# Kernel tuning notes

Hardware: AMD Instinct MI355X
Metric: run time of the kernel (lower is better)

## Reference

```python
import jax, jax.numpy as jnp
import numpy as np

SEQ, B, IN, H = 2048, 4096, 1, 32


def setup_inputs() -> dict:
    key = jax.random.key(0)
    ks = jax.random.split(key, 8)
    s_ih = 1.0 / np.sqrt(H)  # torch nn.RNN init scale
    return {
        "x": jax.random.normal(ks[0], (SEQ, B, IN), dtype=jnp.float32),
        "hidden": jnp.zeros((1, B, H), dtype=jnp.float32),
        "W_ih": jax.random.uniform(ks[1], (H, IN), jnp.float32, -s_ih, s_ih),
        "b_ih": jax.random.uniform(ks[2], (H,), jnp.float32, -s_ih, s_ih),
        "W_hh": jax.random.uniform(ks[3], (H, H), jnp.float32, -s_ih, s_ih),
        "b_hh": jax.random.uniform(ks[4], (H,), jnp.float32, -s_ih, s_ih),
        "W_fc": jax.random.uniform(ks[5], (IN, H), jnp.float32, -s_ih, s_ih),
        "b_fc": jax.random.uniform(ks[6], (IN,), jnp.float32, -s_ih, s_ih),
    }


def reference(x, hidden, W_ih, b_ih, W_hh, b_hh, W_fc, b_fc):
    # Elman RNN: h_t = tanh(x_t W_ih^T + b_ih + h_{t-1} W_hh^T + b_hh)
    # Precompute the input projection for all timesteps in one GEMM.
    x_proj = jnp.einsum('sbi,hi->sbh', x, W_ih) + b_ih + b_hh  # (SEQ, B, H)
    h0 = hidden[0]  # (B, H), single layer

    def step(h, xp_t):
        h_new = jnp.tanh(xp_t + h @ W_hh.T)
        return h_new, h_new

    _, outputs = jax.lax.scan(step, h0, x_proj)  # outputs: (SEQ, B, H)
    # Trailing Linear: (SEQ, B, H) -> (SEQ, B, IN)
    return jnp.einsum('sbh,oh->sbo', outputs, W_fc) + b_fc
```

## Files before the change

kernel.cpp:

```cpp
#include <hip/hip_runtime.h>

#define SEQ   2048
#define BATCH 4096
#define HD    32

__device__ __forceinline__ float exp2_fast(float a) {
#if __has_builtin(__builtin_amdgcn_exp2f)
    return __builtin_amdgcn_exp2f(a);
#else
    return exp2f(a);
#endif
}

__device__ __forceinline__ float rcp_fast(float a) {
#if __has_builtin(__builtin_amdgcn_rcpf)
    return __builtin_amdgcn_rcpf(a);
#else
    return 1.0f / a;
#endif
}

__device__ __forceinline__ float fast_tanh(float v) {
    float ax = fabsf(v);
    float e  = exp2_fast(ax * -2.8853900817779268f);
    float r  = (1.0f - e) * rcp_fast(1.0f + e);
    return copysignf(r, v);
}

template <int CTRL>
__device__ __forceinline__ float dpp_mov0(float v) {
    return __int_as_float(
        __builtin_amdgcn_update_dpp(0, __float_as_int(v), CTRL, 0xF, 0xF, false));
}

__global__ __launch_bounds__(256) void rnn_elman_kernel(
    const float* __restrict__ x, const float* __restrict__ hidden,
    const float* __restrict__ W_ih, const float* __restrict__ b_ih,
    const float* __restrict__ W_hh, const float* __restrict__ b_hh,
    const float* __restrict__ W_fc, const float* __restrict__ b_fc,
    float* __restrict__ out)
{
    __shared__ float sh[16 * 36];

    const int tid = threadIdx.x;
    const int s   = tid & 15;
    const int eb  = tid >> 4;
    const int e   = blockIdx.x * 16 + eb;
    const int r0  = 2 * s;
    const int r1  = 2 * s + 1;

    float4 w0[8], w1[8];
    {
        const float4* W0 = reinterpret_cast<const float4*>(W_hh + r0 * HD);
        const float4* W1 = reinterpret_cast<const float4*>(W_hh + r1 * HD);
        #pragma unroll
        for (int k = 0; k < 8; ++k) { w0[k] = W0[k]; w1[k] = W1[k]; }
    }
    const float wih0  = W_ih[r0], wih1 = W_ih[r1];
    const float bias0 = b_ih[r0] + b_hh[r0];
    const float bias1 = b_ih[r1] + b_hh[r1];
    const float wfc0  = W_fc[r0], wfc1 = W_fc[r1];
    const float bfc   = b_fc[0];

    float* slot = sh + eb * 36;
    reinterpret_cast<float2*>(slot)[s] =
        make_float2(hidden[e * HD + r0], hidden[e * HD + r1]);
    __builtin_amdgcn_wave_barrier();

    float4 hb[8];
    #pragma unroll
    for (int k = 0; k < 8; ++k) hb[k] = reinterpret_cast<const float4*>(slot)[k];

    float xq0 = x[0 * BATCH + e];
    float xq1 = x[1 * BATCH + e];
    float xq2 = x[2 * BATCH + e];
    float xq3 = x[3 * BATCH + e];

    #pragma unroll 4
    for (int t = 0; t < SEQ; ++t) {
        const float xv = xq0;
        xq0 = xq1; xq1 = xq2; xq2 = xq3;
        {
            int tt = t + 4; tt = tt < SEQ - 1 ? tt : SEQ - 1;
            xq3 = x[tt * BATCH + e];
        }

        float a0a = fmaf(xv, wih0, bias0);
        float a1a = fmaf(xv, wih1, bias1);
        float a0b = 0.f, a0c = 0.f, a0d = 0.f;
        float a1b = 0.f, a1c = 0.f, a1d = 0.f;
        #pragma unroll
        for (int k = 0; k < 8; ++k) {
            const float4 h4 = hb[k];
            const float4 ww = w0[k];
            const float4 vv = w1[k];
            a0a = fmaf(ww.x, h4.x, a0a);
            a0b = fmaf(ww.y, h4.y, a0b);
            a0c = fmaf(ww.z, h4.z, a0c);
            a0d = fmaf(ww.w, h4.w, a0d);
            a1a = fmaf(vv.x, h4.x, a1a);
            a1b = fmaf(vv.y, h4.y, a1b);
            a1c = fmaf(vv.z, h4.z, a1c);
            a1d = fmaf(vv.w, h4.w, a1d);
        }
        const float z0 = (a0a + a0b) + (a0c + a0d);
        const float z1 = (a1a + a1b) + (a1c + a1d);

        const float h0 = fast_tanh(z0);
        const float h1 = fast_tanh(z1);

        reinterpret_cast<float2*>(slot)[s] = make_float2(h0, h1);
        __builtin_amdgcn_wave_barrier();
        #pragma unroll
        for (int k = 0; k < 8; ++k) hb[k] = reinterpret_cast<const float4*>(slot)[k];

        float p = fmaf(h0, wfc0, h1 * wfc1);
        p += dpp_mov0<0x111>(p);
        p += dpp_mov0<0x112>(p);
        p += dpp_mov0<0x114>(p);
        p += dpp_mov0<0x118>(p);
        if (s == 15) out[t * BATCH + e] = p + bfc;
    }
}

extern "C" void kernel_launch(void* const* d_in, const int* in_sizes, int n_in,
                              void* d_out, int out_size, void* d_ws, size_t ws_size,
                              hipStream_t stream) {
    const float* x    = (const float*)d_in[0];
    const float* hid  = (const float*)d_in[1];
    const float* W_ih = (const float*)d_in[2];
    const float* b_ih = (const float*)d_in[3];
    const float* W_hh = (const float*)d_in[4];
    const float* b_hh = (const float*)d_in[5];
    const float* W_fc = (const float*)d_in[6];
    const float* b_fc = (const float*)d_in[7];
    float* out = (float*)d_out;

    dim3 grid(BATCH / 16);
    dim3 block(256);
    rnn_elman_kernel<<<grid, block, 0, stream>>>(x, hid, W_ih, b_ih, W_hh, b_hh,
                                                 W_fc, b_fc, out);
}
```

Measured before the change: 592.2 us.

## Exchange RNN hidden state via DPP row rotations instead of LDS

Each 16-lane row now keeps its two hidden values in registers and rotates them across lanes with DPP row_ror. Each lane stores its W_hh columns pre-permuted to match the rotation order. This removes the per-timestep LDS store, wave barrier and vector LDS reloads from the serial recurrence. In exchange it issues 30 cross-lane moves per step, and it also adds a launch-bounds occupancy hint.

```diff
diff --git a/kernel.cpp b/kernel.cpp
--- a/kernel.cpp
+++ b/kernel.cpp
@@ -33,15 +33,13 @@
         __builtin_amdgcn_update_dpp(0, __float_as_int(v), CTRL, 0xF, 0xF, false));
 }
 
-__global__ __launch_bounds__(256) void rnn_elman_kernel(
+__global__ __launch_bounds__(256, 1) void rnn_elman_kernel(
     const float* __restrict__ x, const float* __restrict__ hidden,
     const float* __restrict__ W_ih, const float* __restrict__ b_ih,
     const float* __restrict__ W_hh, const float* __restrict__ b_hh,
     const float* __restrict__ W_fc, const float* __restrict__ b_fc,
     float* __restrict__ out)
 {
-    __shared__ float sh[16 * 36];
-
     const int tid = threadIdx.x;
     const int s   = tid & 15;
     const int eb  = tid >> 4;
@@ -49,12 +47,12 @@
     const int r0  = 2 * s;
     const int r1  = 2 * s + 1;
 
-    float4 w0[8], w1[8];
-    {
-        const float4* W0 = reinterpret_cast<const float4*>(W_hh + r0 * HD);
-        const float4* W1 = reinterpret_cast<const float4*>(W_hh + r1 * HD);
-        #pragma unroll
-        for (int k = 0; k < 8; ++k) { w0[k] = W0[k]; w1[k] = W1[k]; }
+    float2 wr0[16], wr1[16];
+    #pragma unroll
+    for (int i = 0; i < 16; ++i) {
+        const int u = (s - i) & 15;
+        wr0[i] = *reinterpret_cast<const float2*>(W_hh + r0 * HD + 2 * u);
+        wr1[i] = *reinterpret_cast<const float2*>(W_hh + r1 * HD + 2 * u);
     }
     const float wih0  = W_ih[r0], wih1 = W_ih[r1];
     const float bias0 = b_ih[r0] + b_hh[r0];
@@ -62,14 +60,8 @@
     const float wfc0  = W_fc[r0], wfc1 = W_fc[r1];
     const float bfc   = b_fc[0];
 
-    float* slot = sh + eb * 36;
-    reinterpret_cast<float2*>(slot)[s] =
-        make_float2(hidden[e * HD + r0], hidden[e * HD + r1]);
-    __builtin_amdgcn_wave_barrier();
-
-    float4 hb[8];
-    #pragma unroll
-    for (int k = 0; k < 8; ++k) hb[k] = reinterpret_cast<const float4*>(slot)[k];
+    float h0 = hidden[e * HD + r0];
+    float h1 = hidden[e * HD + r1];
 
     float xq0 = x[0 * BATCH + e];
     float xq1 = x[1 * BATCH + e];
@@ -89,30 +81,38 @@
         float a1a = fmaf(xv, wih1, bias1);
         float a0b = 0.f, a0c = 0.f, a0d = 0.f;
         float a1b = 0.f, a1c = 0.f, a1d = 0.f;
-        #pragma unroll
-        for (int k = 0; k < 8; ++k) {
-            const float4 h4 = hb[k];
-            const float4 ww = w0[k];
-            const float4 vv = w1[k];
-            a0a = fmaf(ww.x, h4.x, a0a);
-            a0b = fmaf(ww.y, h4.y, a0b);
-            a0c = fmaf(ww.z, h4.z, a0c);
-            a0d = fmaf(ww.w, h4.w, a0d);
-            a1a = fmaf(vv.x, h4.x, a1a);
-            a1b = fmaf(vv.y, h4.y, a1b);
-            a1c = fmaf(vv.z, h4.z, a1c);
-            a1d = fmaf(vv.w, h4.w, a1d);
+
+        a0a = fmaf(wr0[0].x, h0, a0a);
+        a0b = fmaf(wr0[0].y, h1, a0b);
+        a1a = fmaf(wr1[0].x, h0, a1a);
+        a1b = fmaf(wr1[0].y, h1, a1b);
+
+        #define MV_STEP(i)                                                    \
+        {                                                                     \
+            const float hx = dpp_mov0<0x120 + (i)>(h0);                       \
+            const float hy = dpp_mov0<0x120 + (i)>(h1);                       \
+            if ((i) & 1) {                                                    \
+                a0c = fmaf(wr0[i].x, hx, a0c);                                \
+                a0d = fmaf(wr0[i].y, hy, a0d);                                \
+                a1c = fmaf(wr1[i].x, hx, a1c);                                \
+                a1d = fmaf(wr1[i].y, hy, a1d);                                \
+            } else {                                                          \
+                a0a = fmaf(wr0[i].x, hx, a0a);                                \
+                a0b = fmaf(wr0[i].y, hy, a0b);                                \
+                a1a = fmaf(wr1[i].x, hx, a1a);                                \
+                a1b = fmaf(wr1[i].y, hy, a1b);                                \
+            }                                                                 \
         }
+        MV_STEP(1)  MV_STEP(2)  MV_STEP(3)  MV_STEP(4)  MV_STEP(5)
+        MV_STEP(6)  MV_STEP(7)  MV_STEP(8)  MV_STEP(9)  MV_STEP(10)
+        MV_STEP(11) MV_STEP(12) MV_STEP(13) MV_STEP(14) MV_STEP(15)
+        #undef MV_STEP
+
         const float z0 = (a0a + a0b) + (a0c + a0d);
         const float z1 = (a1a + a1b) + (a1c + a1d);
 
-        const float h0 = fast_tanh(z0);
-        const float h1 = fast_tanh(z1);
-
-        reinterpret_cast<float2*>(slot)[s] = make_float2(h0, h1);
-        __builtin_amdgcn_wave_barrier();
-        #pragma unroll
-        for (int k = 0; k < 8; ++k) hb[k] = reinterpret_cast<const float4*>(slot)[k];
+        h0 = fast_tanh(z0);
+        h1 = fast_tanh(z1);
 
         float p = fmaf(h0, wfc0, h1 * wfc1);
         p += dpp_mov0<0x111>(p);
```

New measurement: 722.4 us. +22.0%, slower.

## Assign one hidden row per lane with 32 lanes per sequence element

Applied to the files above, without the earlier changes.

Each batch element now gets 32 lanes instead of 16, so each lane computes a single hidden unit rather than two. This halves the serial FMA chain per timestep, doubles threads per block to 512, and raises the occupancy hint. The output projection for step t-1 is now reduced at the start of step t, after the shared-memory reads, so it can overlap with the recurrence. That reduction uses mov_dpp with a row broadcast to span 32 lanes. Total VALU work and register demand per wave shift, and the broadcast DPP adds one more dependent step to the reduction.

```diff
diff --git a/kernel.cpp b/kernel.cpp
--- a/kernel.cpp
+++ b/kernel.cpp
@@ -28,12 +28,17 @@
 }
 
 template <int CTRL>
-__device__ __forceinline__ float dpp_mov0(float v) {
+__device__ __forceinline__ float dpp_movf(float v) {
+#if __has_builtin(__builtin_amdgcn_mov_dpp)
+    return __int_as_float(
+        __builtin_amdgcn_mov_dpp(__float_as_int(v), CTRL, 0xF, 0xF, true));
+#else
     return __int_as_float(
         __builtin_amdgcn_update_dpp(0, __float_as_int(v), CTRL, 0xF, 0xF, false));
+#endif
 }
 
-__global__ __launch_bounds__(256) void rnn_elman_kernel(
+__global__ __launch_bounds__(512, 2) void rnn_elman_kernel(
     const float* __restrict__ x, const float* __restrict__ hidden,
     const float* __restrict__ W_ih, const float* __restrict__ b_ih,
     const float* __restrict__ W_hh, const float* __restrict__ b_hh,
@@ -43,33 +48,28 @@
     __shared__ float sh[16 * 36];
 
     const int tid = threadIdx.x;
-    const int s   = tid & 15;
-    const int eb  = tid >> 4;
+    const int s   = tid & 31;
+    const int eb  = tid >> 5;
     const int e   = blockIdx.x * 16 + eb;
-    const int r0  = 2 * s;
-    const int r1  = 2 * s + 1;
 
-    float4 w0[8], w1[8];
+    float4 w[8];
     {
-        const float4* W0 = reinterpret_cast<const float4*>(W_hh + r0 * HD);
-        const float4* W1 = reinterpret_cast<const float4*>(W_hh + r1 * HD);
+        const float4* Wr = reinterpret_cast<const float4*>(W_hh + s * HD);
         #pragma unroll
-        for (int k = 0; k < 8; ++k) { w0[k] = W0[k]; w1[k] = W1[k]; }
+        for (int k = 0; k < 8; ++k) w[k] = Wr[k];
     }
-    const float wih0  = W_ih[r0], wih1 = W_ih[r1];
-    const float bias0 = b_ih[r0] + b_hh[r0];
-    const float bias1 = b_ih[r1] + b_hh[r1];
-    const float wfc0  = W_fc[r0], wfc1 = W_fc[r1];
-    const float bfc   = b_fc[0];
+    const float wih  = W_ih[s];
+    const float bias = b_ih[s] + b_hh[s];
+    const float wfc  = W_fc[s];
+    const float bfc  = b_fc[0];
 
     float* slot = sh + eb * 36;
-    reinterpret_cast<float2*>(slot)[s] =
-        make_float2(hidden[e * HD + r0], hidden[e * HD + r1]);
+    float* wp   = slot + s;
+    const float4* qp = reinterpret_cast<const float4*>(slot);
+
+    float hprev = hidden[e * HD + s];
+    *wp = hprev;
     __builtin_amdgcn_wave_barrier();
-
-    float4 hb[8];
-    #pragma unroll
-    for (int k = 0; k < 8; ++k) hb[k] = reinterpret_cast<const float4*>(slot)[k];
 
     float xq0 = x[0 * BATCH + e];
     float xq1 = x[1 * BATCH + e];
@@ -78,6 +78,25 @@
 
     #pragma unroll 4
     for (int t = 0; t < SEQ; ++t) {
+        const float4 q0 = qp[0];
+        const float4 q1 = qp[1];
+        const float4 q2 = qp[2];
+        const float4 q3 = qp[3];
+        const float4 q4 = qp[4];
+        const float4 q5 = qp[5];
+        const float4 q6 = qp[6];
+        const float4 q7 = qp[7];
+
+        {
+            float p = hprev * wfc;
+            p += dpp_movf<0x111>(p);
+            p += dpp_movf<0x112>(p);
+            p += dpp_movf<0x114>(p);
+            p += dpp_movf<0x118>(p);
+            p += dpp_movf<0x142>(p);
+            if ((t != 0) && (s == 31)) out[(t - 1) * BATCH + e] = p + bfc;
+        }
+
         const float xv = xq0;
         xq0 = xq1; xq1 = xq2; xq2 = xq3;
         {
@@ -85,41 +104,33 @@
             xq3 = x[tt * BATCH + e];
         }
 
-        float a0a = fmaf(xv, wih0, bias0);
-        float a1a = fmaf(xv, wih1, bias1);
-        float a0b = 0.f, a0c = 0.f, a0d = 0.f;
-        float a1b = 0.f, a1c = 0.f, a1d = 0.f;
-        #pragma unroll
-        for (int k = 0; k < 8; ++k) {
-            const float4 h4 = hb[k];
-            const float4 ww = w0[k];
-            const float4 vv = w1[k];
-            a0a = fmaf(ww.x, h4.x, a0a);
-            a0b = fmaf(ww.y, h4.y, a0b);
-            a0c = fmaf(ww.z, h4.z, a0c);
-            a0d = fmaf(ww.w, h4.w, a0d);
-            a1a = fmaf(vv.x, h4.x, a1a);
-            a1b = fmaf(vv.y, h4.y, a1b);
-            a1c = fmaf(vv.z, h4.z, a1c);
-            a1d = fmaf(vv.w, h4.w, a1d);
-        }
-        const float z0 = (a0a + a0b) + (a0c + a0d);
-        const float z1 = (a1a + a1b) + (a1c + a1d);
+        float a0 = fmaf(xv, wih, bias);
+        float a1 = 0.f, a2 = 0.f, a3 = 0.f;
+        #define MV_Q(q, k)                                \
+            a0 = fmaf(w[k].x, (q).x, a0);                 \
+            a1 = fmaf(w[k].y, (q).y, a1);                 \
+            a2 = fmaf(w[k].z, (q).z, a2);                 \
+            a3 = fmaf(w[k].w, (q).w, a3);
+        MV_Q(q0, 0) MV_Q(q1, 1) MV_Q(q2, 2) MV_Q(q3, 3)
+        MV_Q(q4, 4) MV_Q(q5, 5) MV_Q(q6, 6) MV_Q(q7, 7)
+        #undef MV_Q
+        const float z = (a0 + a1) + (a2 + a3);
 
-        const float h0 = fast_tanh(z0);
-        const float h1 = fast_tanh(z1);
+        const float h = fast_tanh(z);
 
-        reinterpret_cast<float2*>(slot)[s] = make_float2(h0, h1);
+        *wp  = h;
+        hprev = h;
         __builtin_amdgcn_wave_barrier();
-        #pragma unroll
-        for (int k = 0; k < 8; ++k) hb[k] = reinterpret_cast<const float4*>(slot)[k];
+    }
 
-        float p = fmaf(h0, wfc0, h1 * wfc1);
-        p += dpp_mov0<0x111>(p);
-        p += dpp_mov0<0x112>(p);
-        p += dpp_mov0<0x114>(p);
-        p += dpp_mov0<0x118>(p);
-        if (s == 15) out[t * BATCH + e] = p + bfc;
+    {
+        float p = hprev * wfc;
+        p += dpp_movf<0x111>(p);
+        p += dpp_movf<0x112>(p);
+        p += dpp_movf<0x114>(p);
+        p += dpp_movf<0x118>(p);
+        p += dpp_movf<0x142>(p);
+        if (s == 31) out[(SEQ - 1) * BATCH + e] = p + bfc;
     }
 }
 
@@ -137,7 +148,7 @@
     float* out = (float*)d_out;
 
     dim3 grid(BATCH / 16);
-    dim3 block(256);
+    dim3 block(512);
     rnn_elman_kernel<<<grid, block, 0, stream>>>(x, hid, W_ih, b_ih, W_hh, b_hh,
                                                  W_fc, b_fc, out);
 }
```

Measured after the change: 671.6 us. +13.4%, slower.
